# Kernel tuning notes

Measured on AMD Instinct MI355X. Metric: run time of the kernel, lower is better.

## Reference

```python
import jax, jax.numpy as jnp
import numpy as np

EMB = 512
N_ROWS = 10000
N_PAIRS = 65536


def setup_inputs() -> dict:
    key = jax.random.key(0)
    ks = jax.random.split(key, 10)
    s1 = 1.0 / np.sqrt(2 * EMB)
    s2 = 1.0 / np.sqrt(128)
    s3 = 1.0 / np.sqrt(64)
    return {
        "pos_pairs": jax.random.randint(ks[0], (N_PAIRS, 3), 0, N_ROWS, dtype=jnp.int32),
        "neg_pairs": jax.random.randint(ks[1], (N_PAIRS, 3), 0, N_ROWS, dtype=jnp.int32),
        "drug_embedding": jax.random.normal(ks[2], (N_ROWS, EMB), dtype=jnp.float32),
        "target_embedding": jax.random.normal(ks[3], (N_ROWS, EMB), dtype=jnp.float32),
        "W1": jax.random.normal(ks[4], (2 * EMB, 128), dtype=jnp.float32) * s1,
        "b1": jnp.zeros((128,), dtype=jnp.float32),
        "W2": jax.random.normal(ks[5], (128, 64), dtype=jnp.float32) * s2,
        "b2": jnp.zeros((64,), dtype=jnp.float32),
        "W3": jax.random.normal(ks[6], (64, 1), dtype=jnp.float32) * s3,
        "b3": jnp.zeros((1,), dtype=jnp.float32),
    }


def _mlp(x, W1, b1, W2, b2, W3, b3):
    h = jax.nn.relu(x @ W1 + b1)
    h = jax.nn.relu(h @ W2 + b2)
    return (h @ W3 + b3)[..., 0]  # [N]


def _pair_loss(pairs, drug_emb, tgt_emb, W1, b1, W2, b2, W3, b3):
    d = drug_emb[pairs[:, 0]]            # [N, EMB]
    t1 = tgt_emb[pairs[:, 1]]            # [N, EMB]
    t2 = tgt_emb[pairs[:, 2]]            # [N, EMB]
    a1 = _mlp(jnp.concatenate([d, t1], axis=-1), W1, b1, W2, b2, W3, b3)
    a2 = _mlp(jnp.concatenate([d, t2], axis=-1), W1, b1, W2, b2, W3, b3)
    # per-pair MSE of scalar affinities = (a1 - a2)^2; mean over pairs
    return jnp.mean((a1 - a2) ** 2)


def reference(pos_pairs, neg_pairs, drug_embedding, target_embedding,
              W1, b1, W2, b2, W3, b3):
    pos = _pair_loss(pos_pairs, drug_embedding, target_embedding, W1, b1, W2, b2, W3, b3)
    neg = _pair_loss(neg_pairs, drug_embedding, target_embedding, W1, b1, W2, b2, W3, b3)
    return pos - neg
```

## Files before the change

kernel.cpp:

```cpp
#include <hip/hip_runtime.h>

#define EMB 512
#define NROWS 10000
#define NPAIRS 65536

typedef __bf16 bf16x8 __attribute__((ext_vector_type(8)));
typedef float  f32x4  __attribute__((ext_vector_type(4)));
typedef unsigned int u32x4 __attribute__((ext_vector_type(4)));

__device__ __forceinline__ void split2(float x0, float x1, unsigned* hw, unsigned* lw) {
    unsigned u0 = __float_as_uint(x0), u1 = __float_as_uint(x1);
    unsigned r0 = u0 + 0x7FFFu + ((u0 >> 16) & 1u);
    unsigned r1 = u1 + 0x7FFFu + ((u1 >> 16) & 1u);
    float h0 = __uint_as_float(r0 & 0xFFFF0000u);
    float h1 = __uint_as_float(r1 & 0xFFFF0000u);
    float l0 = x0 - h0, l1 = x1 - h1;
    unsigned v0 = __float_as_uint(l0), v1 = __float_as_uint(l1);
    unsigned s0 = v0 + 0x7FFFu + ((v0 >> 16) & 1u);
    unsigned s1 = v1 + 0x7FFFu + ((v1 >> 16) & 1u);
    *hw = (r0 >> 16) | (r1 & 0xFFFF0000u);
    *lw = (s0 >> 16) | (s1 & 0xFFFF0000u);
}

__global__ __launch_bounds__(256)
void k0_fragment(const float* __restrict__ W1, const float* __restrict__ W2,
                 unsigned short* __restrict__ W1Fhi, unsigned short* __restrict__ W1Flo,
                 unsigned short* __restrict__ W2Fhi, unsigned short* __restrict__ W2Flo)
{
    int e = blockIdx.x * 256 + threadIdx.x;
    float x;
    unsigned short *hp, *lp;
    if (e < 131072) {
        int i  = e & 7;
        int l  = (e >> 3) & 63;
        int nt = (e >> 9) & 7;
        int kt = (e >> 12) & 15;
        int t  = e >> 16;
        int k = kt * 32 + 8 * (l >> 4) + i;
        int n = nt * 16 + (l & 15);
        x = W1[(t * 512 + k) * 128 + n];
        hp = W1Fhi + e; lp = W1Flo + e;
    } else {
        int e2 = e - 131072;
        int i  = e2 & 7;
        int l  = (e2 >> 3) & 63;
        int nt = (e2 >> 9) & 3;
        int kt = e2 >> 11;
        int k = kt * 32 + 8 * (l >> 4) + i;
        int n = nt * 16 + (l & 15);
        x = W2[k * 64 + n];
        hp = W2Fhi + e2; lp = W2Flo + e2;
    }
    unsigned u = __float_as_uint(x);
    unsigned r = u + 0x7FFFu + ((u >> 16) & 1u);
    float hf = __uint_as_float(r & 0xFFFF0000u);
    float lf = x - hf;
    unsigned v = __float_as_uint(lf);
    unsigned s = v + 0x7FFFu + ((v >> 16) & 1u);
    *hp = (unsigned short)(r >> 16);
    *lp = (unsigned short)(s >> 16);
}

#define K1_RT 313

__global__ __launch_bounds__(256)
void k1_mfma(const float* __restrict__ drug, const float* __restrict__ tgt,
             const unsigned* __restrict__ W1Fhi, const unsigned* __restrict__ W1Flo,
             const float* __restrict__ b1,
             float* __restrict__ D, float* __restrict__ T)
{
    __shared__ float Abuf[32 * 512];

    int bid = blockIdx.x, tid = threadIdx.x;
    bool isT = bid >= K1_RT;
    int rt = isT ? bid - K1_RT : bid;
    const float* emb = isT ? tgt : drug;
    float* out = isT ? T : D;
    int row0 = rt * 32;

    int wave = tid >> 6, lane = tid & 63;
    int g = lane >> 4, lm = lane & 15;
    int mt = wave & 1, nh = wave >> 1;

    #pragma unroll
    for (int it = 0; it < 16; it++) {
        int pr = wave * 8 + (it >> 1);
        int srow = row0 + pr;
        if (srow > NROWS - 1) srow = NROWS - 1;
        int c = (it & 1) * 64 + lane;
        int sc = (c & ~7) | ((lane & 7) ^ (pr & 7));
        __builtin_amdgcn_global_load_lds(
            (const __attribute__((address_space(1))) void*)(emb + (size_t)srow * EMB + sc * 4),
            (__attribute__((address_space(3))) void*)((char*)Abuf + wave * 16384 + it * 1024),
            16, 0, 0);
    }
    __syncthreads();

    const u32x4* BH = (const u32x4*)W1Fhi + (isT ? 8192 : 0);
    const u32x4* BL = (const u32x4*)W1Flo + (isT ? 8192 : 0);
    const f32x4* A4 = (const f32x4*)Abuf;

    int r = mt * 16 + lm, rk = r & 7;

    f32x4 acc[4];
    #pragma unroll
    for (int j = 0; j < 4; j++) { acc[j][0]=0.f; acc[j][1]=0.f; acc[j][2]=0.f; acc[j][3]=0.f; }

    #pragma unroll 4
    for (int kt = 0; kt < 16; kt++) {
        u32x4 bh[4], bl[4];
        #pragma unroll
        for (int j = 0; j < 4; j++) {
            int nt = nh * 4 + j;
            bh[j] = BH[(kt * 8 + nt) * 64 + lane];
            bl[j] = BL[(kt * 8 + nt) * 64 + lane];
        }
        f32x4 a0 = A4[r * 128 + kt * 8 + ((2 * g)     ^ rk)];
        f32x4 a1 = A4[r * 128 + kt * 8 + ((2 * g + 1) ^ rk)];
        unsigned h0, h1, h2, h3, l0, l1, l2, l3;
        split2(a0[0], a0[1], &h0, &l0);
        split2(a0[2], a0[3], &h1, &l1);
        split2(a1[0], a1[1], &h2, &l2);
        split2(a1[2], a1[3], &h3, &l3);
        u32x4 ah, al;
        ah[0]=h0; ah[1]=h1; ah[2]=h2; ah[3]=h3;
        al[0]=l0; al[1]=l1; al[2]=l2; al[3]=l3;
        bf16x8 Ah = __builtin_bit_cast(bf16x8, ah);
        bf16x8 Al = __builtin_bit_cast(bf16x8, al);
        #pragma unroll
        for (int j = 0; j < 4; j++) {
            bf16x8 Bh = __builtin_bit_cast(bf16x8, bh[j]);
            bf16x8 Bl = __builtin_bit_cast(bf16x8, bl[j]);
            acc[j] = __builtin_amdgcn_mfma_f32_16x16x32_bf16(Ah, Bh, acc[j], 0, 0, 0);
            acc[j] = __builtin_amdgcn_mfma_f32_16x16x32_bf16(Ah, Bl, acc[j], 0, 0, 0);
            acc[j] = __builtin_amdgcn_mfma_f32_16x16x32_bf16(Al, Bh, acc[j], 0, 0, 0);
        }
    }

    #pragma unroll
    for (int j = 0; j < 4; j++) {
        int col = (nh * 4 + j) * 16 + lm;
        float bias = isT ? 0.f : b1[col];
        #pragma unroll
        for (int reg = 0; reg < 4; reg++) {
            int row = row0 + mt * 16 + 4 * g + reg;
            if (row < NROWS) out[row * 128 + col] = acc[j][reg] + bias;
        }
    }
}

__global__ __launch_bounds__(256)
void k2_pairs(const float* __restrict__ D, const float* __restrict__ T,
              const int* __restrict__ pos, const int* __restrict__ neg,
              const unsigned* __restrict__ W2Fhi, const unsigned* __restrict__ W2Flo,
              const float* __restrict__ b2, const float* __restrict__ W3,
              double* __restrict__ partials)
{
    __shared__ u32x4 Ash[4][768];

    int tid = threadIdx.x;
    int wave = tid >> 6, lane = tid & 63;
    int g = lane >> 4, lm = lane & 15;
    int rr = lane >> 3, cc = lane & 7;
    int gw = blockIdx.x * 4 + wave;
    const int* pairs = (gw < 2048) ? pos : neg;
    int p0 = (gw & 2047) * 32;

    const float* bp[12];
    #pragma unroll
    for (int it = 0; it < 12; it++) {
        int pr = it * 8 + rr;
        int idxv;
        const float* src;
        if (pr < 32) { idxv = pairs[(p0 + pr) * 3]; src = D; }
        else { int q = pr - 32; idxv = pairs[(p0 + (q >> 1)) * 3 + 1 + (q & 1)]; src = T; }
        bp[it] = src + (size_t)idxv * 128 + ((cc ^ (pr & 7)) << 2);
    }

    u32x4* A4w = &Ash[wave][0];
    const u32x4* BH4 = (const u32x4*)W2Fhi;
    const u32x4* BL4 = (const u32x4*)W2Flo;

    f32x4 acc[4][4];
    #pragma unroll
    for (int mt = 0; mt < 4; mt++)
        #pragma unroll
        for (int nt = 0; nt < 4; nt++) { acc[mt][nt][0]=0.f; acc[mt][nt][1]=0.f; acc[mt][nt][2]=0.f; acc[mt][nt][3]=0.f; }

    #pragma unroll 1
    for (int kt = 0; kt < 4; kt++) {
        u32x4 bh[4], bl[4];
        #pragma unroll
        for (int nt = 0; nt < 4; nt++) {
            bh[nt] = BH4[(kt * 4 + nt) * 64 + lane];
            bl[nt] = BL4[(kt * 4 + nt) * 64 + lane];
        }
        #pragma unroll
        for (int it = 0; it < 12; it++) {
            __builtin_amdgcn_global_load_lds(
                (const __attribute__((address_space(1))) void*)(bp[it] + kt * 32),
                (__attribute__((address_space(3))) void*)((char*)A4w + it * 1024),
                16, 0, 0);
        }
        asm volatile("s_waitcnt vmcnt(0)" ::: "memory");
        #pragma unroll
        for (int mt = 0; mt < 4; mt++) {
            int r = mt * 16 + lm;
            int p = r >> 1;
            int ds = p & 7, ts = r & 7;
            const f32x4* drow = (const f32x4*)(A4w + p * 8);
            const f32x4* trow = (const f32x4*)(A4w + (32 + r) * 8);
            f32x4 d0 = drow[(2 * g) ^ ds];
            f32x4 d1 = drow[(2 * g + 1) ^ ds];
            f32x4 t0 = trow[(2 * g) ^ ts];
            f32x4 t1 = trow[(2 * g + 1) ^ ts];
            float h0 = fmaxf(d0[0] + t0[0], 0.f), h1v = fmaxf(d0[1] + t0[1], 0.f);
            float h2 = fmaxf(d0[2] + t0[2], 0.f), h3 = fmaxf(d0[3] + t0[3], 0.f);
            float h4 = fmaxf(d1[0] + t1[0], 0.f), h5 = fmaxf(d1[1] + t1[1], 0.f);
            float h6 = fmaxf(d1[2] + t1[2], 0.f), h7 = fmaxf(d1[3] + t1[3], 0.f);
            unsigned hq0, hq1, hq2, hq3, lq0, lq1, lq2, lq3;
            split2(h0, h1v, &hq0, &lq0);
            split2(h2, h3,  &hq1, &lq1);
            split2(h4, h5,  &hq2, &lq2);
            split2(h6, h7,  &hq3, &lq3);
            u32x4 ah, al;
            ah[0]=hq0; ah[1]=hq1; ah[2]=hq2; ah[3]=hq3;
            al[0]=lq0; al[1]=lq1; al[2]=lq2; al[3]=lq3;
            bf16x8 Ah = __builtin_bit_cast(bf16x8, ah);
            bf16x8 Al = __builtin_bit_cast(bf16x8, al);
            #pragma unroll
            for (int nt = 0; nt < 4; nt++) {
                bf16x8 Bh = __builtin_bit_cast(bf16x8, bh[nt]);
                bf16x8 Bl = __builtin_bit_cast(bf16x8, bl[nt]);
                acc[mt][nt] = __builtin_amdgcn_mfma_f32_16x16x32_bf16(Ah, Bh, acc[mt][nt], 0, 0, 0);
                acc[mt][nt] = __builtin_amdgcn_mfma_f32_16x16x32_bf16(Ah, Bl, acc[mt][nt], 0, 0, 0);
                acc[mt][nt] = __builtin_amdgcn_mfma_f32_16x16x32_bf16(Al, Bh, acc[mt][nt], 0, 0, 0);
            }
        }
        asm volatile("s_waitcnt lgkmcnt(0)" ::: "memory");
    }

    float b2v[4], w3v[4];
    #pragma unroll
    for (int nt = 0; nt < 4; nt++) { b2v[nt] = b2[nt * 16 + lm]; w3v[nt] = W3[nt * 16 + lm]; }

    float pr[4][4];
    #pragma unroll
    for (int mt = 0; mt < 4; mt++)
        #pragma unroll
        for (int reg = 0; reg < 4; reg++) {
            float s = 0.f;
            #pragma unroll
            for (int nt = 0; nt < 4; nt++) {
                float h2 = fmaxf(acc[mt][nt][reg] + b2v[nt], 0.f);
                s = fmaf(h2, w3v[nt], s);
            }
            pr[mt][reg] = s;
        }
    #pragma unroll
    for (int m = 1; m <= 8; m <<= 1)
        #pragma unroll
        for (int mt = 0; mt < 4; mt++)
            #pragma unroll
            for (int reg = 0; reg < 4; reg++)
                pr[mt][reg] += __shfl_xor(pr[mt][reg], m, 64);

    double dsq = 0.0;
    #pragma unroll
    for (int mt = 0; mt < 4; mt++) {
        float d0 = pr[mt][0] - pr[mt][1];
        float d1 = pr[mt][2] - pr[mt][3];
        dsq += (double)d0 * (double)d0 + (double)d1 * (double)d1;
    }
    dsq += __shfl_xor(dsq, 16, 64);
    dsq += __shfl_xor(dsq, 32, 64);

    __syncthreads();
    if (lane == 0) ((double*)&Ash[wave][0])[0] = dsq;
    __syncthreads();
    if (tid == 0) {
        double sum = 0.0;
        #pragma unroll
        for (int w = 0; w < 4; w++) sum += ((double*)&Ash[w][0])[0];
        partials[blockIdx.x] = sum;
    }
}

__global__ void k3_final(const double* __restrict__ partials, float* __restrict__ out)
{
    int lane = threadIdx.x;
    double sp = 0.0, sn = 0.0;
    #pragma unroll
    for (int i = 0; i < 8; i++) {
        sp += partials[lane + 64 * i];
        sn += partials[512 + lane + 64 * i];
    }
    #pragma unroll
    for (int m = 1; m <= 32; m <<= 1) {
        sp += __shfl_xor(sp, m, 64);
        sn += __shfl_xor(sn, m, 64);
    }
    if (lane == 0) out[0] = (float)((sp - sn) / (double)NPAIRS);
}

extern "C" void kernel_launch(void* const* d_in, const int* in_sizes, int n_in,
                              void* d_out, int out_size, void* d_ws, size_t ws_size,
                              hipStream_t stream) {
    const int*   pos  = (const int*)d_in[0];
    const int*   neg  = (const int*)d_in[1];
    const float* drug = (const float*)d_in[2];
    const float* tgt  = (const float*)d_in[3];
    const float* W1   = (const float*)d_in[4];
    const float* b1   = (const float*)d_in[5];
    const float* W2   = (const float*)d_in[6];
    const float* b2   = (const float*)d_in[7];
    const float* W3   = (const float*)d_in[8];

    float* Dp = (float*)d_ws;
    float* Tp = Dp + NROWS * 128;
    char* base = (char*)(Tp + NROWS * 128);
    unsigned short* W2Fhi = (unsigned short*)base;
    unsigned short* W2Flo = W2Fhi + 8192;
    unsigned short* W1Fhi = W2Flo + 8192;
    unsigned short* W1Flo = W1Fhi + 131072;
    double* partials = (double*)(W1Flo + 131072);
    float* out = (float*)d_out;

    k0_fragment<<<544, 256, 0, stream>>>(W1, W2, W1Fhi, W1Flo, W2Fhi, W2Flo);
    k1_mfma<<<2 * K1_RT, 256, 0, stream>>>(drug, tgt, (const unsigned*)W1Fhi,
                                           (const unsigned*)W1Flo, b1, Dp, Tp);
    k2_pairs<<<1024, 256, 0, stream>>>(Dp, Tp, pos, neg, (const unsigned*)W2Fhi,
                                       (const unsigned*)W2Flo, b2, W3, partials);
    k3_final<<<1, 64, 0, stream>>>(partials, out);
}
```

Baseline: 65.55 us.

## Retile projection GEMM to 128-row blocks with K-chunked LDS staging

Restructures the per-row W1 projection kernel from 32-row, 256-thread blocks to 128-row, 512-thread blocks. Each wave now computes a 64x32 output tile and loops over four K chunks, staging 128 columns of the embedding rows in LDS per chunk. This cuts how often the W1 hi/lo fragments are re-read from global memory, since each B fragment is reused across four M tiles. In exchange it launches only 158 blocks, fewer than the GPU's CU count, and adds per-chunk barriers with no overlap between loads and compute.

Measured after the change: 71.16 us. +8.6%, slower.

```diff
diff --git a/kernel.cpp b/kernel.cpp
--- a/kernel.cpp
+++ b/kernel.cpp
@@ -61,91 +61,105 @@
     *lp = (unsigned short)(s >> 16);
 }
 
-#define K1_RT 313
-
-__global__ __launch_bounds__(256)
+#define K1_BLOCKS 79
+
+__global__ __launch_bounds__(512)
 void k1_mfma(const float* __restrict__ drug, const float* __restrict__ tgt,
              const unsigned* __restrict__ W1Fhi, const unsigned* __restrict__ W1Flo,
              const float* __restrict__ b1,
              float* __restrict__ D, float* __restrict__ T)
 {
-    __shared__ float Abuf[32 * 512];
+    __shared__ float Abuf[4][128][32];
 
     int bid = blockIdx.x, tid = threadIdx.x;
-    bool isT = bid >= K1_RT;
-    int rt = isT ? bid - K1_RT : bid;
+    bool isT = bid >= K1_BLOCKS;
+    int rt = isT ? bid - K1_BLOCKS : bid;
     const float* emb = isT ? tgt : drug;
     float* out = isT ? T : D;
-    int row0 = rt * 32;
+    int row0 = rt * 128;
 
     int wave = tid >> 6, lane = tid & 63;
     int g = lane >> 4, lm = lane & 15;
-    int mt = wave & 1, nh = wave >> 1;
-
-    #pragma unroll
-    for (int it = 0; it < 16; it++) {
-        int pr = wave * 8 + (it >> 1);
-        int srow = row0 + pr;
-        if (srow > NROWS - 1) srow = NROWS - 1;
-        int c = (it & 1) * 64 + lane;
-        int sc = (c & ~7) | ((lane & 7) ^ (pr & 7));
-        __builtin_amdgcn_global_load_lds(
-            (const __attribute__((address_space(1))) void*)(emb + (size_t)srow * EMB + sc * 4),
-            (__attribute__((address_space(3))) void*)((char*)Abuf + wave * 16384 + it * 1024),
-            16, 0, 0);
-    }
-    __syncthreads();
+    int mw = wave & 1, nw = wave >> 1;
 
     const u32x4* BH = (const u32x4*)W1Fhi + (isT ? 8192 : 0);
     const u32x4* BL = (const u32x4*)W1Flo + (isT ? 8192 : 0);
-    const f32x4* A4 = (const f32x4*)Abuf;
-
-    int r = mt * 16 + lm, rk = r & 7;
-
-    f32x4 acc[4];
-    #pragma unroll
-    for (int j = 0; j < 4; j++) { acc[j][0]=0.f; acc[j][1]=0.f; acc[j][2]=0.f; acc[j][3]=0.f; }
-
-    #pragma unroll 4
-    for (int kt = 0; kt < 16; kt++) {
-        u32x4 bh[4], bl[4];
-        #pragma unroll
-        for (int j = 0; j < 4; j++) {
-            int nt = nh * 4 + j;
-            bh[j] = BH[(kt * 8 + nt) * 64 + lane];
-            bl[j] = BL[(kt * 8 + nt) * 64 + lane];
-        }
-        f32x4 a0 = A4[r * 128 + kt * 8 + ((2 * g)     ^ rk)];
-        f32x4 a1 = A4[r * 128 + kt * 8 + ((2 * g + 1) ^ rk)];
-        unsigned h0, h1, h2, h3, l0, l1, l2, l3;
-        split2(a0[0], a0[1], &h0, &l0);
-        split2(a0[2], a0[3], &h1, &l1);
-        split2(a1[0], a1[1], &h2, &l2);
-        split2(a1[2], a1[3], &h3, &l3);
-        u32x4 ah, al;
-        ah[0]=h0; ah[1]=h1; ah[2]=h2; ah[3]=h3;
-        al[0]=l0; al[1]=l1; al[2]=l2; al[3]=l3;
-        bf16x8 Ah = __builtin_bit_cast(bf16x8, ah);
-        bf16x8 Al = __builtin_bit_cast(bf16x8, al);
-        #pragma unroll
-        for (int j = 0; j < 4; j++) {
-            bf16x8 Bh = __builtin_bit_cast(bf16x8, bh[j]);
-            bf16x8 Bl = __builtin_bit_cast(bf16x8, bl[j]);
-            acc[j] = __builtin_amdgcn_mfma_f32_16x16x32_bf16(Ah, Bh, acc[j], 0, 0, 0);
-            acc[j] = __builtin_amdgcn_mfma_f32_16x16x32_bf16(Ah, Bl, acc[j], 0, 0, 0);
-            acc[j] = __builtin_amdgcn_mfma_f32_16x16x32_bf16(Al, Bh, acc[j], 0, 0, 0);
-        }
-    }
-
-    #pragma unroll
-    for (int j = 0; j < 4; j++) {
-        int col = (nh * 4 + j) * 16 + lm;
+
+    f32x4 acc[4][2];
+    #pragma unroll
+    for (int mt = 0; mt < 4; mt++)
+        #pragma unroll
+        for (int j = 0; j < 2; j++) { acc[mt][j][0]=0.f; acc[mt][j][1]=0.f; acc[mt][j][2]=0.f; acc[mt][j][3]=0.f; }
+
+    #pragma unroll 1
+    for (int kq = 0; kq < 4; kq++) {
+        #pragma unroll
+        for (int i = 0; i < 8; i++) {
+            int it  = wave * 8 + i;
+            int ktl = it >> 4;
+            int r8  = (it & 15) * 8 + (lane >> 3);
+            int ch  = lane & 7;
+            int srow = row0 + r8;
+            if (srow > NROWS - 1) srow = NROWS - 1;
+            int sch = ch ^ (r8 & 7);
+            __builtin_amdgcn_global_load_lds(
+                (const __attribute__((address_space(1))) void*)
+                    (emb + (size_t)srow * EMB + kq * 128 + ktl * 32 + sch * 4),
+                (__attribute__((address_space(3))) void*)((char*)Abuf + it * 1024),
+                16, 0, 0);
+        }
+        __syncthreads();
+        #pragma unroll
+        for (int ktl = 0; ktl < 4; ktl++) {
+            int ktg = kq * 4 + ktl;
+            u32x4 bh[2], bl[2];
+            #pragma unroll
+            for (int j = 0; j < 2; j++) {
+                int nt = nw * 2 + j;
+                bh[j] = BH[(ktg * 8 + nt) * 64 + lane];
+                bl[j] = BL[(ktg * 8 + nt) * 64 + lane];
+            }
+            const f32x4* slab = (const f32x4*)&Abuf[ktl][0][0];
+            #pragma unroll
+            for (int mt = 0; mt < 4; mt++) {
+                int r = mw * 64 + mt * 16 + lm, rk = r & 7;
+                f32x4 a0 = slab[r * 8 + ((2 * g)     ^ rk)];
+                f32x4 a1 = slab[r * 8 + ((2 * g + 1) ^ rk)];
+                unsigned h0, h1, h2, h3, l0, l1, l2, l3;
+                split2(a0[0], a0[1], &h0, &l0);
+                split2(a0[2], a0[3], &h1, &l1);
+                split2(a1[0], a1[1], &h2, &l2);
+                split2(a1[2], a1[3], &h3, &l3);
+                u32x4 ah, al;
+                ah[0]=h0; ah[1]=h1; ah[2]=h2; ah[3]=h3;
+                al[0]=l0; al[1]=l1; al[2]=l2; al[3]=l3;
+                bf16x8 Ah = __builtin_bit_cast(bf16x8, ah);
+                bf16x8 Al = __builtin_bit_cast(bf16x8, al);
+                #pragma unroll
+                for (int j = 0; j < 2; j++) {
+                    bf16x8 Bh = __builtin_bit_cast(bf16x8, bh[j]);
+                    bf16x8 Bl = __builtin_bit_cast(bf16x8, bl[j]);
+                    acc[mt][j] = __builtin_amdgcn_mfma_f32_16x16x32_bf16(Ah, Bh, acc[mt][j], 0, 0, 0);
+                    acc[mt][j] = __builtin_amdgcn_mfma_f32_16x16x32_bf16(Ah, Bl, acc[mt][j], 0, 0, 0);
+                    acc[mt][j] = __builtin_amdgcn_mfma_f32_16x16x32_bf16(Al, Bh, acc[mt][j], 0, 0, 0);
+                }
+            }
+        }
+        asm volatile("s_waitcnt lgkmcnt(0)" ::: "memory");
+        __syncthreads();
+    }
+
+    #pragma unroll
+    for (int j = 0; j < 2; j++) {
+        int col = (nw * 2 + j) * 16 + lm;
         float bias = isT ? 0.f : b1[col];
         #pragma unroll
-        for (int reg = 0; reg < 4; reg++) {
-            int row = row0 + mt * 16 + 4 * g + reg;
-            if (row < NROWS) out[row * 128 + col] = acc[j][reg] + bias;
-        }
+        for (int mt = 0; mt < 4; mt++)
+            #pragma unroll
+            for (int reg = 0; reg < 4; reg++) {
+                int row = row0 + mw * 64 + mt * 16 + 4 * g + reg;
+                if (row < NROWS) out[row * 128 + col] = acc[mt][j][reg] + bias;
+            }
     }
 }
 
@@ -327,8 +341,8 @@
     float* out = (float*)d_out;
 
     k0_fragment<<<544, 256, 0, stream>>>(W1, W2, W1Fhi, W1Flo, W2Fhi, W2Flo);
-    k1_mfma<<<2 * K1_RT, 256, 0, stream>>>(drug, tgt, (const unsigned*)W1Fhi,
-                                           (const unsigned*)W1Flo, b1, Dp, Tp);
+    k1_mfma<<<2 * K1_BLOCKS, 512, 0, stream>>>(drug, tgt, (const unsigned*)W1Fhi,
+                                               (const unsigned*)W1Flo, b1, Dp, Tp);
     k2_pairs<<<1024, 256, 0, stream>>>(Dp, Tp, pos, neg, (const unsigned*)W2Fhi,
                                        (const unsigned*)W2Flo, b2, W3, partials);
     k3_final<<<1, 64, 0, stream>>>(partials, out);
```
